# Performance work log

Measured on AMD Instinct MI355X. Metric: run time of the kernel, lower is better.

## Reference

```python
import jax, jax.numpy as jnp
import numpy as np
import math

N, D, W, R = 131072, 128, 16, 5


def setup_inputs() -> dict:
    key = jax.random.key(0)
    k1, k2, k3, k4, k5 = jax.random.split(key, 5)
    stdv = 1.0 / math.sqrt(R)
    return {
        "embeds1": jax.random.normal(k1, (N, D), dtype=jnp.float32),
        "embeds2": jax.random.normal(k2, (N, D), dtype=jnp.float32),
        "rel_embeds": jax.random.normal(k3, (W, D * D), dtype=jnp.float32),
        "weight_scalars": jax.random.uniform(k4, (W, R), dtype=jnp.float32, minval=-stdv, maxval=stdv),
        "rels": jax.random.randint(k5, (N,), 0, R, dtype=jnp.int64),
    }


def reference(embeds1, embeds2, rel_embeds, weight_scalars, rels):
    n, d = embeds1.shape
    w, r = weight_scalars.shape
    rel_mats = rel_embeds.reshape(w, d, d)  # [W, D, D] per-basis bilinear matrices
    # basis_outputs[n, w] = embeds1[n] @ rel_mats[w] @ embeds2[n]
    basis_outputs = jnp.einsum('nd,wde,ne->nw', embeds1, rel_mats, embeds2)
    logit = basis_outputs @ weight_scalars            # [N, R]
    outputs = jax.nn.log_softmax(logit, axis=1)       # [N, R]
    # NLLLoss(mean) on log-probs gathered at the true relation
    log_probs = jnp.take_along_axis(outputs, rels[:, None], axis=1)  # [N, 1]
    loss = -log_probs.mean()
    # preds = sum_j (j+1) * p_j  (expected rating), shape [N, 1]
    ratings = jnp.arange(1, r + 1, dtype=outputs.dtype)
    preds = (jnp.exp(outputs) @ ratings)[:, None]
    return loss, preds
```

## Files before the change

### kernel.cpp

```cpp
#include <hip/hip_runtime.h>
#include <stdint.h>


#define NTOT 131072
#define DDIM 128
#define WBAS 16
#define RCLS 5
#define BN   64
#define SA   144
#define NBLK (NTOT / BN)

typedef __attribute__((ext_vector_type(8))) short bf16x8;
typedef __attribute__((ext_vector_type(4))) float f32x4;

__device__ __forceinline__ unsigned short f2bf(float x) {
    union { float f; unsigned u; } v; v.f = x;
    unsigned u = v.u + 0x7FFFu + ((v.u >> 16) & 1u);
    return (unsigned short)(u >> 16);
}

__global__ __launch_bounds__(256) void prep_kernel(
    const float* __restrict__ rel_embeds,
    const float* __restrict__ wsc,
    unsigned short* __restrict__ Cth)
{
    __shared__ float tile[8][129];
    const int bx = blockIdx.x;
    const int r  = bx >> 4;
    const int d0 = (bx & 15) << 3;
    const int t  = threadIdx.x;

    const int e  = t & 127;
    const int dl = t >> 7;

    float acc[4] = {0.f, 0.f, 0.f, 0.f};
    for (int w = 0; w < WBAS; ++w) {
        float s = wsc[w * RCLS + r];
#pragma unroll
        for (int dd = 0; dd < 4; ++dd)
            acc[dd] += s * rel_embeds[w * 16384 + (d0 + dd * 2 + dl) * 128 + e];
    }
#pragma unroll
    for (int dd = 0; dd < 4; ++dd) tile[dd * 2 + dl][e] = acc[dd];
    __syncthreads();

    if (t < 128) {
        unsigned short h[8];
#pragma unroll
        for (int j = 0; j < 8; ++j) h[j] = f2bf(tile[j][t]);
        size_t base = (size_t)r * 16384 + (size_t)t * 128 + d0;
        *(ushort4*)(Cth + base)     = make_ushort4(h[0], h[1], h[2], h[3]);
        *(ushort4*)(Cth + base + 4) = make_ushort4(h[4], h[5], h[6], h[7]);
    }
}

__global__ __launch_bounds__(256, 3) void bilinear_mfma_kernel(
    const float* __restrict__ e1g,
    const float* __restrict__ e2g,
    const unsigned short* __restrict__ Cth,
    const int*   __restrict__ rels,
    float* __restrict__ out,
    float* __restrict__ loss_ws,
    float inv_n)
{
    __shared__ __align__(16) unsigned short s_hi[BN][SA];
    __shared__ float s_part[4][BN][RCLS];

    const int tid  = threadIdx.x;
    const int n0   = blockIdx.x * BN;
    const int lane = tid & 63;
    const int w    = tid >> 6;
    const int l15  = lane & 15;
    const int q    = lane >> 4;

    f32x4 e2r[2][4];
#pragma unroll
    for (int nt = 0; nt < 4; ++nt) {
        const float* p = e2g + (size_t)(n0 + 16 * nt + l15) * DDIM + 32 * w + 4 * q;
        e2r[0][nt] = *(const f32x4*)p;
        e2r[1][nt] = *(const f32x4*)(p + 16);
    }

#pragma unroll
    for (int it = 0; it < 8; ++it) {
        int idx = it * 256 + tid;
        int row = idx >> 5, c4 = idx & 31;
        float4 v = ((const float4*)(e1g + (size_t)(n0 + row) * DDIM))[c4];
        *(ushort4*)&s_hi[row][c4 * 4] =
            make_ushort4(f2bf(v.x), f2bf(v.y), f2bf(v.z), f2bf(v.w));
    }
    __syncthreads();

    const int aofs0 = (32 * w + l15) * DDIM + q * 8;
    const int aofs1 = aofs0 + 16 * DDIM;

    const unsigned short* ag = Cth;

#pragma unroll 1
    for (int r = 0; r < RCLS; ++r) {
        f32x4 acc[2][4];
#pragma unroll
        for (int et = 0; et < 2; ++et)
#pragma unroll
            for (int nt = 0; nt < 4; ++nt) {
                f32x4 z = {0.0f, 0.0f, 0.0f, 0.0f};
                acc[et][nt] = z;
            }

#pragma unroll
        for (int k4 = 0; k4 < 4; ++k4) {
            bf16x8 a0 = *(const bf16x8*)(ag + aofs0 + k4 * 32);
            bf16x8 a1 = *(const bf16x8*)(ag + aofs1 + k4 * 32);
            bf16x8 bh[4];
#pragma unroll
            for (int nt = 0; nt < 4; ++nt)
                bh[nt] = *(const bf16x8*)&s_hi[16 * nt + l15][k4 * 32 + q * 8];
#pragma unroll
            for (int nt = 0; nt < 4; ++nt) {
                acc[0][nt] = __builtin_amdgcn_mfma_f32_16x16x32_bf16(a0, bh[nt], acc[0][nt], 0, 0, 0);
                acc[1][nt] = __builtin_amdgcn_mfma_f32_16x16x32_bf16(a1, bh[nt], acc[1][nt], 0, 0, 0);
            }
        }

#pragma unroll
        for (int nt = 0; nt < 4; ++nt) {
            f32x4 t = acc[0][nt] * e2r[0][nt] + acc[1][nt] * e2r[1][nt];
            float p = t[0] + t[1] + t[2] + t[3];
            p += __shfl_xor(p, 16);
            p += __shfl_xor(p, 32);
            if (lane < 16) s_part[w][16 * nt + lane][r] = p;
        }

        ag += 16384;
    }
    __syncthreads();

    if (tid < BN) {
        float l[RCLS];
#pragma unroll
        for (int r = 0; r < RCLS; ++r)
            l[r] = s_part[0][tid][r] + s_part[1][tid][r]
                 + s_part[2][tid][r] + s_part[3][tid][r];
        float mx = l[0];
#pragma unroll
        for (int r = 1; r < RCLS; ++r) mx = fmaxf(mx, l[r]);
        float e[RCLS], se = 0.0f;
#pragma unroll
        for (int r = 0; r < RCLS; ++r) { e[r] = __expf(l[r] - mx); se += e[r]; }
        float inv_se = 1.0f / se;
        float pred = 0.0f;
#pragma unroll
        for (int r = 0; r < RCLS; ++r) pred += (float)(r + 1) * e[r] * inv_se;
        out[1 + n0 + tid] = pred;

        int rel = rels[n0 + tid];
        float lossc = -(l[rel] - mx - logf(se)) * inv_n;
#pragma unroll
        for (int m = 1; m <= 32; m <<= 1) lossc += __shfl_xor(lossc, m);
        if (lane == 0) loss_ws[blockIdx.x] = lossc;
    }
}

__global__ __launch_bounds__(256) void loss_reduce_kernel(
    const float* __restrict__ loss_ws, float* __restrict__ out)
{
    __shared__ float s[4];
    float v = 0.0f;
    for (int i = threadIdx.x; i < NBLK; i += 256) v += loss_ws[i];
#pragma unroll
    for (int m = 1; m <= 32; m <<= 1) v += __shfl_xor(v, m);
    if ((threadIdx.x & 63) == 0) s[threadIdx.x >> 6] = v;
    __syncthreads();
    if (threadIdx.x == 0) out[0] = s[0] + s[1] + s[2] + s[3];
}

extern "C" void kernel_launch(void* const* d_in, const int* in_sizes, int n_in,
                              void* d_out, int out_size, void* d_ws, size_t ws_size,
                              hipStream_t stream) {
    const float* e1   = (const float*)d_in[0];
    const float* e2   = (const float*)d_in[1];
    const float* rele = (const float*)d_in[2];
    const float* wsc  = (const float*)d_in[3];
    const int*   rels = (const int*)d_in[4];
    float* out = (float*)d_out;

    unsigned short* Cth = (unsigned short*)d_ws;
    float* loss_ws = (float*)((char*)d_ws + 163840);

    prep_kernel<<<80, 256, 0, stream>>>(rele, wsc, Cth);
    bilinear_mfma_kernel<<<NBLK, 256, 0, stream>>>(
        e1, e2, Cth, rels, out, loss_ws, 1.0f / (float)NTOT);
    loss_reduce_kernel<<<1, 256, 0, stream>>>(loss_ws, out);
}
```

Measured before the change: 191.7 us.

## Make bilinear kernel persistent with double-buffered prefetch of next embeds1 tile

The main kernel now launches a fixed grid of 1024 blocks, each looping over two 64-row groups instead of one block per group. The next group's embeds1 rows are loaded into registers and converted to bf16 into a second LDS buffer, interleaved with the MFMA class loop, so global latency overlaps compute. This costs twice the LDS for both the tile and partial-sum buffers plus extra prefetch registers, which may lower occupancy under the 3-blocks-per-CU bound, and with only two iterations per block the overlap is limited.

New measurement: 197.3 us. 1.03x slower.

```diff
diff --git a/kernel.cpp b/kernel.cpp
--- a/kernel.cpp
+++ b/kernel.cpp
@@ -8,7 +8,8 @@
 #define RCLS 5
 #define BN   64
 #define SA   144
-#define NBLK (NTOT / BN)
+#define NG   (NTOT / BN)
+#define GRID 1024
 
 typedef __attribute__((ext_vector_type(8))) short bf16x8;
 typedef __attribute__((ext_vector_type(4))) float f32x4;
@@ -17,6 +18,10 @@
     union { float f; unsigned u; } v; v.f = x;
     unsigned u = v.u + 0x7FFFu + ((v.u >> 16) & 1u);
     return (unsigned short)(u >> 16);
+}
+
+__device__ __forceinline__ ushort4 f2bf4(float4 v) {
+    return make_ushort4(f2bf(v.x), f2bf(v.y), f2bf(v.z), f2bf(v.w));
 }
 
 __global__ __launch_bounds__(256) void prep_kernel(
@@ -63,101 +68,136 @@
     float* __restrict__ loss_ws,
     float inv_n)
 {
-    __shared__ __align__(16) unsigned short s_hi[BN][SA];
-    __shared__ float s_part[4][BN][RCLS];
+    __shared__ __align__(16) unsigned short s_hi[2][BN][SA];
+    __shared__ float s_part[2][4][BN][RCLS];
 
     const int tid  = threadIdx.x;
-    const int n0   = blockIdx.x * BN;
     const int lane = tid & 63;
     const int w    = tid >> 6;
     const int l15  = lane & 15;
     const int q    = lane >> 4;
-
-    f32x4 e2r[2][4];
-#pragma unroll
-    for (int nt = 0; nt < 4; ++nt) {
-        const float* p = e2g + (size_t)(n0 + 16 * nt + l15) * DDIM + 32 * w + 4 * q;
-        e2r[0][nt] = *(const f32x4*)p;
-        e2r[1][nt] = *(const f32x4*)(p + 16);
-    }
-
-#pragma unroll
-    for (int it = 0; it < 8; ++it) {
-        int idx = it * 256 + tid;
-        int row = idx >> 5, c4 = idx & 31;
-        float4 v = ((const float4*)(e1g + (size_t)(n0 + row) * DDIM))[c4];
-        *(ushort4*)&s_hi[row][c4 * 4] =
-            make_ushort4(f2bf(v.x), f2bf(v.y), f2bf(v.z), f2bf(v.w));
-    }
-    __syncthreads();
-
+    const int sr0  = tid >> 5;
+    const int sc4  = tid & 31;
+
+    const int bofs  = l15 * SA + q * 8;
     const int aofs0 = (32 * w + l15) * DDIM + q * 8;
     const int aofs1 = aofs0 + 16 * DDIM;
 
-    const unsigned short* ag = Cth;
-
+    int g = blockIdx.x;
+    int b = 0;
+
+    {
+        const float* e1b = e1g + (size_t)g * BN * DDIM;
+        float4 v[8];
+#pragma unroll
+        for (int it = 0; it < 8; ++it)
+            v[it] = *(const float4*)(e1b + (it * 8 + sr0) * DDIM + sc4 * 4);
+#pragma unroll
+        for (int it = 0; it < 8; ++it)
+            *(ushort4*)&s_hi[0][it * 8 + sr0][sc4 * 4] = f2bf4(v[it]);
+    }
+    __syncthreads();
+
+    for (; g < NG; g += GRID) {
+        const int n0 = g * BN;
+        const int gn = g + GRID;
+        const float* e1n = e1g + (size_t)gn * BN * DDIM;
+        const unsigned short* sb = &s_hi[b][0][0];
+        unsigned short*       sn = &s_hi[b ^ 1][0][0];
+
+        f32x4 e2r[2][4];
+#pragma unroll
+        for (int nt = 0; nt < 4; ++nt) {
+            const float* pp = e2g + (size_t)(n0 + 16 * nt + l15) * DDIM + 32 * w + 4 * q;
+            e2r[0][nt] = *(const f32x4*)pp;
+            e2r[1][nt] = *(const f32x4*)(pp + 16);
+        }
+
+        float4 pf[4];
+        if (gn < NG) {
+#pragma unroll
+            for (int it = 0; it < 4; ++it)
+                pf[it] = *(const float4*)(e1n + (it * 8 + sr0) * DDIM + sc4 * 4);
+        }
+
+        const unsigned short* ag = Cth;
 #pragma unroll 1
-    for (int r = 0; r < RCLS; ++r) {
-        f32x4 acc[2][4];
-#pragma unroll
-        for (int et = 0; et < 2; ++et)
+        for (int r = 0; r < RCLS; ++r) {
+            f32x4 acc[2][4];
+#pragma unroll
+            for (int et = 0; et < 2; ++et)
+#pragma unroll
+                for (int nt = 0; nt < 4; ++nt) {
+                    f32x4 z = {0.0f, 0.0f, 0.0f, 0.0f};
+                    acc[et][nt] = z;
+                }
+
+#pragma unroll
+            for (int k4 = 0; k4 < 4; ++k4) {
+                bf16x8 a0 = *(const bf16x8*)(ag + aofs0 + k4 * 32);
+                bf16x8 a1 = *(const bf16x8*)(ag + aofs1 + k4 * 32);
+                bf16x8 bh[4];
+#pragma unroll
+                for (int nt = 0; nt < 4; ++nt)
+                    bh[nt] = *(const bf16x8*)(sb + bofs + nt * (16 * SA) + k4 * 32);
+#pragma unroll
+                for (int nt = 0; nt < 4; ++nt) {
+                    acc[0][nt] = __builtin_amdgcn_mfma_f32_16x16x32_bf16(a0, bh[nt], acc[0][nt], 0, 0, 0);
+                    acc[1][nt] = __builtin_amdgcn_mfma_f32_16x16x32_bf16(a1, bh[nt], acc[1][nt], 0, 0, 0);
+                }
+            }
+
 #pragma unroll
             for (int nt = 0; nt < 4; ++nt) {
-                f32x4 z = {0.0f, 0.0f, 0.0f, 0.0f};
-                acc[et][nt] = z;
+                f32x4 t = acc[0][nt] * e2r[0][nt] + acc[1][nt] * e2r[1][nt];
+                float p2 = t[0] + t[1] + t[2] + t[3];
+                p2 += __shfl_xor(p2, 16);
+                p2 += __shfl_xor(p2, 32);
+                if (lane < 16) s_part[b][w][16 * nt + lane][r] = p2;
             }
 
-#pragma unroll
-        for (int k4 = 0; k4 < 4; ++k4) {
-            bf16x8 a0 = *(const bf16x8*)(ag + aofs0 + k4 * 32);
-            bf16x8 a1 = *(const bf16x8*)(ag + aofs1 + k4 * 32);
-            bf16x8 bh[4];
-#pragma unroll
-            for (int nt = 0; nt < 4; ++nt)
-                bh[nt] = *(const bf16x8*)&s_hi[16 * nt + l15][k4 * 32 + q * 8];
-#pragma unroll
-            for (int nt = 0; nt < 4; ++nt) {
-                acc[0][nt] = __builtin_amdgcn_mfma_f32_16x16x32_bf16(a0, bh[nt], acc[0][nt], 0, 0, 0);
-                acc[1][nt] = __builtin_amdgcn_mfma_f32_16x16x32_bf16(a1, bh[nt], acc[1][nt], 0, 0, 0);
+            if (r == 1 && gn < NG) {
+#pragma unroll
+                for (int it = 0; it < 4; ++it)
+                    *(ushort4*)(sn + (it * 8 + sr0) * SA + sc4 * 4) = f2bf4(pf[it]);
+#pragma unroll
+                for (int it = 0; it < 4; ++it)
+                    pf[it] = *(const float4*)(e1n + ((it + 4) * 8 + sr0) * DDIM + sc4 * 4);
+            } else if (r == 3 && gn < NG) {
+#pragma unroll
+                for (int it = 0; it < 4; ++it)
+                    *(ushort4*)(sn + ((it + 4) * 8 + sr0) * SA + sc4 * 4) = f2bf4(pf[it]);
             }
-        }
-
-#pragma unroll
-        for (int nt = 0; nt < 4; ++nt) {
-            f32x4 t = acc[0][nt] * e2r[0][nt] + acc[1][nt] * e2r[1][nt];
-            float p = t[0] + t[1] + t[2] + t[3];
-            p += __shfl_xor(p, 16);
-            p += __shfl_xor(p, 32);
-            if (lane < 16) s_part[w][16 * nt + lane][r] = p;
-        }
-
-        ag += 16384;
-    }
-    __syncthreads();
-
-    if (tid < BN) {
-        float l[RCLS];
-#pragma unroll
-        for (int r = 0; r < RCLS; ++r)
-            l[r] = s_part[0][tid][r] + s_part[1][tid][r]
-                 + s_part[2][tid][r] + s_part[3][tid][r];
-        float mx = l[0];
-#pragma unroll
-        for (int r = 1; r < RCLS; ++r) mx = fmaxf(mx, l[r]);
-        float e[RCLS], se = 0.0f;
-#pragma unroll
-        for (int r = 0; r < RCLS; ++r) { e[r] = __expf(l[r] - mx); se += e[r]; }
-        float inv_se = 1.0f / se;
-        float pred = 0.0f;
-#pragma unroll
-        for (int r = 0; r < RCLS; ++r) pred += (float)(r + 1) * e[r] * inv_se;
-        out[1 + n0 + tid] = pred;
-
-        int rel = rels[n0 + tid];
-        float lossc = -(l[rel] - mx - logf(se)) * inv_n;
-#pragma unroll
-        for (int m = 1; m <= 32; m <<= 1) lossc += __shfl_xor(lossc, m);
-        if (lane == 0) loss_ws[blockIdx.x] = lossc;
+
+            ag += 16384;
+        }
+        __syncthreads();
+
+        if (tid < BN) {
+            float l[RCLS];
+#pragma unroll
+            for (int r = 0; r < RCLS; ++r)
+                l[r] = s_part[b][0][tid][r] + s_part[b][1][tid][r]
+                     + s_part[b][2][tid][r] + s_part[b][3][tid][r];
+            float mx = l[0];
+#pragma unroll
+            for (int r = 1; r < RCLS; ++r) mx = fmaxf(mx, l[r]);
+            float e[RCLS], se = 0.0f;
+#pragma unroll
+            for (int r = 0; r < RCLS; ++r) { e[r] = __expf(l[r] - mx); se += e[r]; }
+            float inv_se = 1.0f / se;
+            float pred = 0.0f;
+#pragma unroll
+            for (int r = 0; r < RCLS; ++r) pred += (float)(r + 1) * e[r] * inv_se;
+            out[1 + n0 + tid] = pred;
+
+            int rel = rels[n0 + tid];
+            float lossc = -(l[rel] - mx - logf(se)) * inv_n;
+#pragma unroll
+            for (int m = 1; m <= 32; m <<= 1) lossc += __shfl_xor(lossc, m);
+            if (lane == 0) loss_ws[g] = lossc;
+        }
+        b ^= 1;
     }
 }
 
@@ -166,7 +206,7 @@
 {
     __shared__ float s[4];
     float v = 0.0f;
-    for (int i = threadIdx.x; i < NBLK; i += 256) v += loss_ws[i];
+    for (int i = threadIdx.x; i < NG; i += 256) v += loss_ws[i];
 #pragma unroll
     for (int m = 1; m <= 32; m <<= 1) v += __shfl_xor(v, m);
     if ((threadIdx.x & 63) == 0) s[threadIdx.x >> 6] = v;
@@ -188,7 +228,7 @@
     float* loss_ws = (float*)((char*)d_ws + 163840);
 
     prep_kernel<<<80, 256, 0, stream>>>(rele, wsc, Cth);
-    bilinear_mfma_kernel<<<NBLK, 256, 0, stream>>>(
+    bilinear_mfma_kernel<<<GRID, 256, 0, stream>>>(
         e1, e2, Cth, rels, out, loss_ws, 1.0f / (float)NTOT);
     loss_reduce_kernel<<<1, 256, 0, stream>>>(loss_ws, out);
 }
```
